# Performance work log

Measured on AMD Instinct MI355X. Metric: run time of the kernel, lower is better.

Reference implementation:

```python
import jax, jax.numpy as jnp
import numpy as np

L, D, H, IMG, P, B, E = 12, 768, 12, 224, 16, 32, 512
HD = D // H            # 64
FF = 4 * D             # 3072
SEQ = (IMG // P) ** 2 + 1  # 197


def _ln(x, w, b, eps=1e-5):
    m = x.mean(-1, keepdims=True)
    v = jnp.mean((x - m) ** 2, axis=-1, keepdims=True)
    return (x - m) * jax.lax.rsqrt(v + eps) * w + b


def setup_inputs() -> dict:
    key = jax.random.key(0)
    ks = jax.random.split(key, 10)
    r = lambda k, shape, s=0.02: (jax.random.normal(k, shape, jnp.float32) * s)
    return {
        'image': jax.random.normal(ks[0], (B, 3, IMG, IMG), jnp.float32),
        'conv_w': r(ks[1], (D, 3, P, P)),
        'cls_emb': r(ks[2], (D,)),
        'pos_emb': r(ks[3], (SEQ, D)),
        'ln_pre_w': jnp.ones((D,), jnp.float32), 'ln_pre_b': jnp.zeros((D,), jnp.float32),
        'ln1_w': jnp.ones((L, D), jnp.float32), 'ln1_b': jnp.zeros((L, D), jnp.float32),
        'qkv_w': r(ks[4], (L, 3 * D, D)), 'qkv_b': jnp.zeros((L, 3 * D), jnp.float32),
        'out_w': r(ks[5], (L, D, D)), 'out_b': jnp.zeros((L, D), jnp.float32),
        'ln2_w': jnp.ones((L, D), jnp.float32), 'ln2_b': jnp.zeros((L, D), jnp.float32),
        'fc_w': r(ks[6], (L, FF, D)), 'fc_b': jnp.zeros((L, FF), jnp.float32),
        'pr_w': r(ks[7], (L, D, FF)), 'pr_b': jnp.zeros((L, D), jnp.float32),
        'ln_post_w': jnp.ones((D,), jnp.float32), 'ln_post_b': jnp.zeros((D,), jnp.float32),
        'proj': r(ks[8], (D, E)),
    }


def reference(image, conv_w, cls_emb, pos_emb, ln_pre_w, ln_pre_b,
              ln1_w, ln1_b, qkv_w, qkv_b, out_w, out_b,
              ln2_w, ln2_b, fc_w, fc_b, pr_w, pr_b,
              ln_post_w, ln_post_b, proj):
    # patchify: conv stride=kernel=patch, no bias -> [B, D, 14, 14]
    x = jax.lax.conv_general_dilated(image, conv_w, (P, P), 'VALID',
                                     dimension_numbers=('NCHW', 'OIHW', 'NCHW'))
    x = x.reshape(B, D, -1).transpose(0, 2, 1)               # [B, 196, D]
    cls = jnp.broadcast_to(cls_emb, (B, 1, D))
    x = jnp.concatenate([cls, x], axis=1) + pos_emb          # [B, SEQ, D]
    x = _ln(x, ln_pre_w, ln_pre_b)
    x = x.transpose(1, 0, 2)                                  # [SEQ, B, D]
    scale = 1.0 / np.sqrt(HD).astype(np.float32)

    def step(x, p):
        l1w, l1b, qw, qb, ow, ob, l2w, l2b, fw, fb, pw, pb = p
        h = _ln(x, l1w, l1b)
        qkv = h @ qw.T + qb                                    # [SEQ, B, 3D]
        q, k, v = jnp.split(qkv, 3, axis=-1)
        heads = lambda t: t.reshape(SEQ, B * H, HD).transpose(1, 0, 2)  # [B*H, SEQ, HD]
        q = heads(q) * scale
        k = heads(k)
        v = heads(v)
        a = jax.nn.softmax(jnp.einsum('nsh,nth->nst', q, k), axis=-1)   # [B*H, SEQ, SEQ]
        o = jnp.einsum('nst,nth->nsh', a, v)                  # [B*H, SEQ, HD]
        o = o.transpose(1, 0, 2).reshape(SEQ, B, D)
        x = x + (o @ ow.T + ob)
        h = _ln(x, l2w, l2b)
        h = jax.nn.gelu(h @ fw.T + fb, approximate=False)      # torch nn.GELU (exact)
        x = x + (h @ pw.T + pb)
        return x, None

    x, _ = jax.lax.scan(step, x, (ln1_w, ln1_b, qkv_w, qkv_b, out_w, out_b,
                                  ln2_w, ln2_b, fc_w, fc_b, pr_w, pr_b))
    x = x.transpose(1, 0, 2)                                   # [B, SEQ, D]
    cls_tok = _ln(x[:, 0, :], ln_post_w, ln_post_b)
    feats = cls_tok @ proj                                     # [B, E]
    return feats / jnp.linalg.norm(feats, axis=-1, keepdims=True)
```

## Files before the change

kernel.cpp:

```cpp
#include <hip/hip_runtime.h>
#include <stdint.h>

#define SEQ 197
#define NB 32
#define NH 12
#define NTOK (SEQ*NB)
#define MPAD 6400
#define NPATCH 6272

typedef unsigned short u16;
typedef unsigned int u32;
typedef __attribute__((ext_vector_type(8))) short bv8;
typedef __attribute__((ext_vector_type(4))) float f32x4;

__device__ __forceinline__ u16 f2bf(float f){
  u32 u = __float_as_uint(f);
  u = (u + 0x7fffu + ((u >> 16) & 1u)) >> 16;
  return (u16)u;
}
__device__ __forceinline__ float bf2f(u16 h){ return __uint_as_float(((u32)h) << 16); }

#if defined(__has_builtin)
#if __has_builtin(__builtin_amdgcn_global_load_lds)
#define HAS_GLLDS 1
#endif
#endif

__device__ __forceinline__ void gl_lds16(const void* g, void* l){
#ifdef HAS_GLLDS
  __builtin_amdgcn_global_load_lds(
      (const __attribute__((address_space(1))) void*)(uintptr_t)g,
      (__attribute__((address_space(3))) void*)(u32)(uintptr_t)l, 16, 0, 0);
#else
  int lane = threadIdx.x & 63;
  uint4 v = *(const uint4*)((const char*)g);
  *(uint4*)((char*)l + lane*16) = v;
#endif
}

__device__ __forceinline__ void red2(float& a, float& b){
  #pragma unroll
  for (int o = 32; o > 0; o >>= 1){ a += __shfl_down(a, o); b += __shfl_down(b, o); }
  __shared__ float red[8];
  int w = threadIdx.x >> 6, ln = threadIdx.x & 63;
  if (ln == 0){ red[w] = a; red[4 + w] = b; }
  __syncthreads();
  a = red[0] + red[1] + red[2] + red[3];
  b = red[4] + red[5] + red[6] + red[7];
}

__global__ __launch_bounds__(256) void cvt_k(const float* __restrict__ src, u16* __restrict__ dst, int n4){
  int i = blockIdx.x * 256 + threadIdx.x;
  if (i >= n4) return;
  float4 f = ((const float4*)src)[i];
  u32 lo = (u32)f2bf(f.x) | ((u32)f2bf(f.y) << 16);
  u32 hi = (u32)f2bf(f.z) | ((u32)f2bf(f.w) << 16);
  ((uint2*)dst)[i] = make_uint2(lo, hi);
}

__global__ __launch_bounds__(256) void im2col_k(const float* __restrict__ img, u16* __restrict__ Ap){
  int gid = blockIdx.x * 256 + threadIdx.x;
  int row = gid / 768, k = gid - row * 768;
  int b = row / 196, p = row - b * 196;
  int pr = p / 14, pc = p - pr * 14;
  int c = k >> 8, r = k & 255;
  int ph = r >> 4, pw = r & 15;
  size_t src = ((size_t)(b * 3 + c) * 224 + (pr * 16 + ph)) * 224 + (pc * 16 + pw);
  Ap[gid] = f2bf(img[src]);
}

template<int EPI>
__global__ __launch_bounds__(256, 2)
void gemm_2ph(const u16* __restrict__ A, const u16* __restrict__ Bw,
              const float* __restrict__ bias, float* __restrict__ Cf,
              u16* __restrict__ Cb, int N, int K, int Mreal,
              int RM, int RN, int tmT, int tnT)
{
  __shared__ __align__(16) u16 sA0[128 * 64];
  __shared__ __align__(16) u16 sB0[128 * 64];
  __shared__ __align__(16) u16 sA1[128 * 64];
  __shared__ __align__(16) u16 sB1[128 * 64];
  const int xcd = blockIdx.x & 7, pos = blockIdx.x >> 3;
  const int xm = xcd >> 1, xn = xcd & 1;
  const int tm = xm * RM + pos / RN;
  const int tn = xn * RN + pos % RN;
  if (tm >= tmT || tn >= tnT) return;

  const int tid = threadIdx.x;
  const int lane = tid & 63, wave = tid >> 6;
  const int wm = wave >> 1, wn = wave & 1;
  const int lr = lane & 15, g = lane >> 4, g4 = g * 4;
  const int KT = K >> 6;

  const int srow = lane >> 3;
  const int sch = (lane & 7) ^ srow;
  const u16* aB[4]; const u16* bB[4];
  #pragma unroll
  for (int j = 0; j < 4; j++){
    int rr = wave * 32 + j * 8;
    aB[j] = A  + (size_t)(tm * 128 + rr + srow) * K + sch * 8;
    bB[j] = Bw + (size_t)(tn * 128 + rr + srow) * K + sch * 8;
  }

  f32x4 acc[4][4] = {};

  auto stage = [&](int kt, u16* dA, u16* dB){
    #pragma unroll
    for (int j = 0; j < 4; j++)
      gl_lds16(aB[j] + (size_t)kt * 64, dA + (wave * 32 + j * 8) * 64);
    #pragma unroll
    for (int j = 0; j < 4; j++)
      gl_lds16(bB[j] + (size_t)kt * 64, dB + (wave * 32 + j * 8) * 64);
  };
  auto tile = [&](const u16* sA, const u16* sB, u16* dA, u16* dB, int ktNext, bool doStage, bool last){
    if (last) asm volatile("s_waitcnt vmcnt(0)" ::: "memory");
    else      asm volatile("s_waitcnt vmcnt(8)" ::: "memory");
    __builtin_amdgcn_s_barrier();
    bv8 af[4][2], bf[4][2];
    #pragma unroll
    for (int mi = 0; mi < 4; mi++){
      int row = wm * 64 + mi * 16 + lr;
      #pragma unroll
      for (int kk = 0; kk < 2; kk++)
        af[mi][kk] = *(const bv8*)((const char*)sA + row * 128 + ((kk * 64 + g * 16) ^ ((row & 7) << 4)));
    }
    #pragma unroll
    for (int ni = 0; ni < 4; ni++){
      int row = wn * 64 + ni * 16 + lr;
      #pragma unroll
      for (int kk = 0; kk < 2; kk++)
        bf[ni][kk] = *(const bv8*)((const char*)sB + row * 128 + ((kk * 64 + g * 16) ^ ((row & 7) << 4)));
    }
    asm volatile("s_waitcnt lgkmcnt(0)" ::: "memory");
    __builtin_amdgcn_s_barrier();
    if (doStage) stage(ktNext, dA, dB);
    __builtin_amdgcn_s_setprio(1);
    #pragma unroll
    for (int kk = 0; kk < 2; kk++)
      #pragma unroll
      for (int mi = 0; mi < 4; mi++)
        #pragma unroll
        for (int ni = 0; ni < 4; ni++)
          acc[mi][ni] = __builtin_amdgcn_mfma_f32_16x16x32_bf16(af[mi][kk], bf[ni][kk], acc[mi][ni], 0, 0, 0);
    __builtin_amdgcn_s_setprio(0);
  };

  stage(0, sA0, sB0);
  stage(1, sA1, sB1);
  int t = 0;
  for (; t + 2 < KT; t += 2){
    tile(sA0, sB0, sA0, sB0, t + 2, true,  false);
    tile(sA1, sB1, sA1, sB1, t + 3, true,  false);
  }
  tile(sA0, sB0, sA0, sB0, 0, false, false);
  tile(sA1, sB1, sA1, sB1, 0, false, true);

  if (EPI == 1 || EPI == 3){
    __syncthreads();
    #pragma unroll
    for (int mi = 0; mi < 4; mi++){
      #pragma unroll
      for (int ni = 0; ni < 4; ni++){
        int bcol = wn * 64 + ni * 16 + lr;
        float bvs = bias[tn * 128 + bcol];
        #pragma unroll
        for (int j = 0; j < 4; j++){
          int brow = wm * 64 + mi * 16 + g4 + j;
          float v = acc[mi][ni][j] + bvs;
          if (EPI == 3) v = 0.5f * v * (1.f + erff(v * 0.70710678118654752f));
          char* base = (char*)(brow < 64 ? sA0 : sB0);
          *(u16*)(base + (brow & 63) * 256 + ((bcol * 2) ^ ((brow & 7) << 4))) = f2bf(v);
        }
      }
    }
    __syncthreads();
    #pragma unroll
    for (int c = 0; c < 8; c++){
      int off = c * 4096 + tid * 16;
      int row = off >> 8;
      int colb = off & 255;
      const char* base = (const char*)(row < 64 ? sA0 : sB0);
      uint4 v = *(const uint4*)(base + (row & 63) * 256 + (colb ^ ((row & 7) << 4)));
      *(uint4*)((char*)(Cb + (size_t)(tm * 128 + row) * N + tn * 128) + colb) = v;
    }
  } else {
    #pragma unroll
    for (int ni = 0; ni < 4; ni++){
      int col = tn * 128 + wn * 64 + ni * 16 + lr;
      float bvs = (EPI != 0) ? bias[col] : 0.f;
      #pragma unroll
      for (int mi = 0; mi < 4; mi++){
        int row0 = tm * 128 + wm * 64 + mi * 16 + g4;
        #pragma unroll
        for (int j = 0; j < 4; j++){
          int row = row0 + j;
          if (row < Mreal){
            float v = acc[mi][ni][j] + bvs;
            size_t idx = (size_t)row * N + col;
            if (EPI == 0) Cf[idx] = v;
            else          Cf[idx] += v;
          }
        }
      }
    }
  }
}

__global__ __launch_bounds__(256, 1) void attn_k(const u16* __restrict__ qkv, u16* __restrict__ o_out){
  __shared__ __align__(16) u16 sK[256 * 64];
  __shared__ __align__(16) u16 sVT[64 * 256];
  __shared__ __align__(16) u16 sP[4 * 64 * 64];
  const int bh = blockIdx.x;
  const int b = bh / NH, h = bh - b * NH;
  const int tid = threadIdx.x;
  const int lane = tid & 63, wave = tid >> 6;
  const int lr = lane & 15, g = lane >> 4;
  const int g4 = g * 4;
  const int wb = wave * 64;
  const u16* kbase = qkv + (size_t)b * SEQ * 2304 + h * 64 + 768;
  const u16* vbase = kbase + 768;

  bv8 qf[4][2];
  #pragma unroll
  for (int qt = 0; qt < 4; qt++){
    int q = wb + qt * 16 + lr; if (q > 196) q = 196;
    const u16* qr = qkv + (size_t)(b * SEQ + q) * 2304 + h * 64;
    #pragma unroll
    for (int kc = 0; kc < 2; kc++)
      qf[qt][kc] = *(const bv8*)(qr + kc * 32 + g * 8);
  }

  for (int i = tid; i < 197 * 32; i += 256){
    int r = i >> 5, c = i & 31;
    u32 kv_ = *(const u32*)(kbase + (size_t)r * 2304 + c * 2);
    *(u32*)((char*)sK + ((r * 128 + c * 4) ^ ((r & 7) << 4))) = kv_;
    u32 vv = *(const u32*)(vbase + (size_t)r * 2304 + c * 2);
    int hd0 = c * 2, hd1 = c * 2 + 1;
    *(u16*)((char*)sVT + ((hd0 * 512 + r * 2) ^ ((hd0 & 7) << 4))) = (u16)(vv & 0xffff);
    *(u16*)((char*)sVT + ((hd1 * 512 + r * 2) ^ ((hd1 & 7) << 4))) = (u16)(vv >> 16);
  }
  for (int i = tid; i < 59 * 32; i += 256){
    int r = 197 + (i >> 5), c = i & 31;
    *(u32*)((char*)sK + (r * 128 + c * 4)) = 0;
  }
  for (int i = tid; i < 59 * 64; i += 256){
    int kv = 197 + (i >> 6), hd = i & 63;
    *(u16*)((char*)sVT + ((hd * 512 + kv * 2) ^ ((hd & 7) << 4))) = 0;
  }
  __syncthreads();

  f32x4 acc_o[4][4] = {};
  float m_[4] = {-1e30f, -1e30f, -1e30f, -1e30f};
  float l_[4] = {0.f, 0.f, 0.f, 0.f};
  u16* sPw = sP + wave * 4096;

  for (int ch = 0; ch < 4; ++ch){
    f32x4 st[4][4] = {};
    #pragma unroll
    for (int kc = 0; kc < 2; kc++){
      bv8 kf[4];
      #pragma unroll
      for (int kvt = 0; kvt < 4; kvt++){
        int row = ch * 64 + kvt * 16 + lr;
        kf[kvt] = *(const bv8*)((const char*)sK + ((row * 128 + kc * 64 + g * 16) ^ ((row & 7) << 4)));
      }
      #pragma unroll
      for (int kvt = 0; kvt < 4; kvt++)
        #pragma unroll
        for (int qt = 0; qt < 4; qt++)
          st[kvt][qt] = __builtin_amdgcn_mfma_f32_16x16x32_bf16(kf[kvt], qf[qt][kc], st[kvt][qt], 0, 0, 0);
    }
    float fac[4];
    #pragma unroll
    for (int qt = 0; qt < 4; qt++){
      float mx = -1e30f;
      #pragma unroll
      for (int kvt = 0; kvt < 4; kvt++)
        #pragma unroll
        for (int j = 0; j < 4; j++){
          int kvg = ch * 64 + kvt * 16 + g4 + j;
          float s = st[kvt][qt][j] * 0.125f;
          s = (kvg < 197) ? s : -1e30f;
          st[kvt][qt][j] = s;
          mx = fmaxf(mx, s);
        }
      mx = fmaxf(mx, __shfl_xor(mx, 16));
      mx = fmaxf(mx, __shfl_xor(mx, 32));
      float nm = fmaxf(m_[qt], mx);
      fac[qt] = __expf(m_[qt] - nm);
      m_[qt] = nm;
      float ls = 0.f;
      #pragma unroll
      for (int kvt = 0; kvt < 4; kvt++)
        #pragma unroll
        for (int j = 0; j < 4; j++){
          float p = __expf(st[kvt][qt][j] - nm);
          st[kvt][qt][j] = p;
          ls += p;
        }
      ls += __shfl_xor(ls, 16);
      ls += __shfl_xor(ls, 32);
      l_[qt] = l_[qt] * fac[qt] + ls;
    }
    #pragma unroll
    for (int qt = 0; qt < 4; qt++)
      #pragma unroll
      for (int j = 0; j < 4; j++){
        float fj = __shfl(fac[qt], (lane & 48) | (g4 + j));
        #pragma unroll
        for (int nt = 0; nt < 4; nt++) acc_o[qt][nt][j] *= fj;
      }
    #pragma unroll
    for (int qt = 0; qt < 4; qt++){
      int row = qt * 16 + lr;
      #pragma unroll
      for (int kvt = 0; kvt < 4; kvt++){
        uint2 pk;
        pk.x = (u32)f2bf(st[kvt][qt][0]) | ((u32)f2bf(st[kvt][qt][1]) << 16);
        pk.y = (u32)f2bf(st[kvt][qt][2]) | ((u32)f2bf(st[kvt][qt][3]) << 16);
        *(uint2*)((char*)sPw + ((row * 128 + kvt * 32 + g * 8) ^ ((row & 7) << 4))) = pk;
      }
    }
    #pragma unroll
    for (int kc = 0; kc < 2; kc++){
      bv8 pa[4], vb[4];
      #pragma unroll
      for (int qt = 0; qt < 4; qt++){
        int row = qt * 16 + lr;
        pa[qt] = *(const bv8*)((const char*)sPw + ((row * 128 + kc * 64 + g * 16) ^ ((row & 7) << 4)));
      }
      #pragma unroll
      for (int nt = 0; nt < 4; nt++){
        int hd = nt * 16 + lr;
        vb[nt] = *(const bv8*)((const char*)sVT + ((hd * 512 + ch * 128 + kc * 64 + g * 16) ^ ((hd & 7) << 4)));
      }
      #pragma unroll
      for (int qt = 0; qt < 4; qt++)
        #pragma unroll
        for (int nt = 0; nt < 4; nt++)
          acc_o[qt][nt] = __builtin_amdgcn_mfma_f32_16x16x32_bf16(pa[qt], vb[nt], acc_o[qt][nt], 0, 0, 0);
    }
  }

  #pragma unroll
  for (int qt = 0; qt < 4; qt++)
    #pragma unroll
    for (int j = 0; j < 4; j++){
      float lj = __shfl(l_[qt], (lane & 48) | (g4 + j));
      float rl = 1.f / lj;
      int row = wb + qt * 16 + g4 + j;
      if (row < 197){
        u16* dst = o_out + (size_t)(b * SEQ + row) * 768 + h * 64;
        #pragma unroll
        for (int nt = 0; nt < 4; nt++)
          dst[nt * 16 + lr] = f2bf(acc_o[qt][nt][j] * rl);
      }
    }
}

__global__ __launch_bounds__(256) void embed_ln_k(const float* __restrict__ patch, const float* __restrict__ cls,
    const float* __restrict__ pos, const float* __restrict__ w, const float* __restrict__ bb, float* __restrict__ x)
{
  int t = blockIdx.x;
  int b = t / SEQ, s = t - b * SEQ;
  int tid = threadIdx.x;
  float v[3];
  #pragma unroll
  for (int i = 0; i < 3; i++){
    int d = tid + i * 256;
    float base = (s == 0) ? cls[d] : patch[(size_t)(b * 196 + s - 1) * 768 + d];
    v[i] = base + pos[s * 768 + d];
  }
  float sm = v[0] + v[1] + v[2];
  float sq = v[0]*v[0] + v[1]*v[1] + v[2]*v[2];
  red2(sm, sq);
  float m = sm * (1.f / 768.f);
  float rs = rsqrtf(sq * (1.f / 768.f) - m * m + 1e-5f);
  #pragma unroll
  for (int i = 0; i < 3; i++){
    int d = tid + i * 256;
    x[(size_t)t * 768 + d] = (v[i] - m) * rs * w[d] + bb[d];
  }
}

__global__ __launch_bounds__(256) void ln_bf16_k(const float* __restrict__ x, const float* __restrict__ w,
    const float* __restrict__ bb, u16* __restrict__ h)
{
  int t = blockIdx.x, tid = threadIdx.x;
  const float* xr = x + (size_t)t * 768;
  float v[3];
  #pragma unroll
  for (int i = 0; i < 3; i++) v[i] = xr[tid + i * 256];
  float sm = v[0] + v[1] + v[2];
  float sq = v[0]*v[0] + v[1]*v[1] + v[2]*v[2];
  red2(sm, sq);
  float m = sm * (1.f / 768.f);
  float rs = rsqrtf(sq * (1.f / 768.f) - m * m + 1e-5f);
  #pragma unroll
  for (int i = 0; i < 3; i++){
    int d = tid + i * 256;
    h[(size_t)t * 768 + d] = f2bf((v[i] - m) * rs * w[d] + bb[d]);
  }
}

__global__ __launch_bounds__(256) void ln_cls_k(const float* __restrict__ x, const float* __restrict__ w,
    const float* __restrict__ bb, float* __restrict__ cls)
{
  int b = blockIdx.x, tid = threadIdx.x;
  const float* xr = x + (size_t)b * SEQ * 768;
  float v[3];
  #pragma unroll
  for (int i = 0; i < 3; i++) v[i] = xr[tid + i * 256];
  float sm = v[0] + v[1] + v[2];
  float sq = v[0]*v[0] + v[1]*v[1] + v[2]*v[2];
  red2(sm, sq);
  float m = sm * (1.f / 768.f);
  float rs = rsqrtf(sq * (1.f / 768.f) - m * m + 1e-5f);
  #pragma unroll
  for (int i = 0; i < 3; i++){
    int d = tid + i * 256;
    cls[b * 768 + d] = (v[i] - m) * rs * w[d] + bb[d];
  }
}

__global__ __launch_bounds__(256) void proj_k(const float* __restrict__ cls, const float* __restrict__ P,
                                              float* __restrict__ feats){
  int gid = blockIdx.x * 256 + threadIdx.x;
  int b = gid >> 9, e = gid & 511;
  const float* c = cls + b * 768;
  float a0 = 0, a1 = 0, a2 = 0, a3 = 0;
  for (int d = 0; d < 768; d += 4){
    a0 += c[d]     * P[(size_t)d * 512 + e];
    a1 += c[d + 1] * P[(size_t)(d + 1) * 512 + e];
    a2 += c[d + 2] * P[(size_t)(d + 2) * 512 + e];
    a3 += c[d + 3] * P[(size_t)(d + 3) * 512 + e];
  }
  feats[gid] = (a0 + a1) + (a2 + a3);
}

__global__ __launch_bounds__(256) void norm_k(const float* __restrict__ feats, float* __restrict__ out){
  int b = blockIdx.x, tid = threadIdx.x;
  float v0 = feats[b * 512 + tid], v1 = feats[b * 512 + 256 + tid];
  float sq = v0 * v0 + v1 * v1, dummy = 0.f;
  red2(sq, dummy);
  float inv = 1.f / sqrtf(sq);
  out[b * 512 + tid] = v0 * inv;
  out[b * 512 + 256 + tid] = v1 * inv;
}

extern "C" void kernel_launch(void* const* d_in, const int* in_sizes, int n_in,
                              void* d_out, int out_size, void* d_ws, size_t ws_size,
                              hipStream_t stream)
{
  const float* image   = (const float*)d_in[0];
  const float* conv_w  = (const float*)d_in[1];
  const float* cls_emb = (const float*)d_in[2];
  const float* pos_emb = (const float*)d_in[3];
  const float* lnprew  = (const float*)d_in[4];
  const float* lnpreb  = (const float*)d_in[5];
  const float* ln1w    = (const float*)d_in[6];
  const float* ln1b    = (const float*)d_in[7];
  const float* qkvw    = (const float*)d_in[8];
  const float* qkvb    = (const float*)d_in[9];
  const float* outw    = (const float*)d_in[10];
  const float* outb    = (const float*)d_in[11];
  const float* ln2w    = (const float*)d_in[12];
  const float* ln2b    = (const float*)d_in[13];
  const float* fcw     = (const float*)d_in[14];
  const float* fcb     = (const float*)d_in[15];
  const float* prw     = (const float*)d_in[16];
  const float* prb     = (const float*)d_in[17];
  const float* lnpostw = (const float*)d_in[18];
  const float* lnpostb = (const float*)d_in[19];
  const float* proj    = (const float*)d_in[20];
  (void)in_sizes; (void)n_in; (void)out_size;

  const size_t QW = (size_t)2304 * 768, OW = (size_t)768 * 768;
  const size_t FW = (size_t)3072 * 768, PW = (size_t)768 * 3072;
  const size_t CW = (size_t)768 * 768;

  char* p = (char*)d_ws;
  auto alloc = [&](size_t bytes)->char*{ char* r = p; p += (bytes + 255) & ~(size_t)255; return r; };
  float* x     = (float*)alloc((size_t)MPAD * 768 * 4);
  u16*   h     = (u16*)  alloc((size_t)MPAD * 768 * 2);
  u16*   qkvB  = (u16*)  alloc((size_t)MPAD * 2304 * 2);
  u16*   attno = (u16*)  alloc((size_t)MPAD * 768 * 2);
  u16*   ffh   = (u16*)  alloc((size_t)MPAD * 3072 * 2);
  u16*   Ap    = (u16*)  alloc((size_t)NPATCH * 768 * 2);
  float* patch = (float*)alloc((size_t)NPATCH * 768 * 4);
  float* clsb  = (float*)alloc((size_t)32 * 768 * 4);
  float* feats = (float*)alloc((size_t)32 * 512 * 4);
  u16*   cwb   = (u16*)  alloc(CW * 2);
  size_t base_used = (size_t)(p - (char*)d_ws);
  size_t full_need = (QW + OW + FW + PW) * 12 * 2;
  bool full = (base_used + full_need + 4096 <= ws_size);

  u16 *wq = nullptr, *wo = nullptr, *wf = nullptr, *wp = nullptr;
  u16 *sq_ = nullptr, *so_ = nullptr, *sf_ = nullptr, *sp_ = nullptr;
  if (full){
    wq = (u16*)alloc(QW * 12 * 2); wo = (u16*)alloc(OW * 12 * 2);
    wf = (u16*)alloc(FW * 12 * 2); wp = (u16*)alloc(PW * 12 * 2);
  } else {
    sq_ = (u16*)alloc(QW * 2); so_ = (u16*)alloc(OW * 2);
    sf_ = (u16*)alloc(FW * 2); sp_ = (u16*)alloc(PW * 2);
  }
  if ((size_t)(p - (char*)d_ws) > ws_size) return;

  { int n4 = (int)(CW / 4); cvt_k<<<(n4 + 255) / 256, 256, 0, stream>>>(conv_w, cwb, n4); }
  if (full){
    int n4;
    n4 = (int)(QW * 12 / 4); cvt_k<<<(n4 + 255) / 256, 256, 0, stream>>>(qkvw, wq, n4);
    n4 = (int)(OW * 12 / 4); cvt_k<<<(n4 + 255) / 256, 256, 0, stream>>>(outw, wo, n4);
    n4 = (int)(FW * 12 / 4); cvt_k<<<(n4 + 255) / 256, 256, 0, stream>>>(fcw,  wf, n4);
    n4 = (int)(PW * 12 / 4); cvt_k<<<(n4 + 255) / 256, 256, 0, stream>>>(prw,  wp, n4);
  }

  im2col_k<<<(NPATCH * 768) / 256, 256, 0, stream>>>(image, Ap);
  gemm_2ph<0><<<8 * 13 * 3, 256, 0, stream>>>(Ap, cwb, nullptr, patch, nullptr, 768, 768, NPATCH, 13, 3, 49, 6);
  embed_ln_k<<<NTOK, 256, 0, stream>>>(patch, cls_emb, pos_emb, lnprew, lnpreb, x);

  for (int l = 0; l < 12; l++){
    const u16 *WQ, *WO, *WF, *WP;
    if (full){
      WQ = wq + (size_t)l * QW; WO = wo + (size_t)l * OW;
      WF = wf + (size_t)l * FW; WP = wp + (size_t)l * PW;
    } else {
      int n4;
      n4 = (int)(QW / 4); cvt_k<<<(n4 + 255) / 256, 256, 0, stream>>>(qkvw + (size_t)l * QW, sq_, n4);
      n4 = (int)(OW / 4); cvt_k<<<(n4 + 255) / 256, 256, 0, stream>>>(outw + (size_t)l * OW, so_, n4);
      n4 = (int)(FW / 4); cvt_k<<<(n4 + 255) / 256, 256, 0, stream>>>(fcw  + (size_t)l * FW, sf_, n4);
      n4 = (int)(PW / 4); cvt_k<<<(n4 + 255) / 256, 256, 0, stream>>>(prw  + (size_t)l * PW, sp_, n4);
      WQ = sq_; WO = so_; WF = sf_; WP = sp_;
    }
    ln_bf16_k<<<NTOK, 256, 0, stream>>>(x, ln1w + l * 768, ln1b + l * 768, h);
    gemm_2ph<1><<<8 * 13 * 9, 256, 0, stream>>>(h, WQ, qkvb + l * 2304, nullptr, qkvB, 2304, 768, NTOK, 13, 9, 50, 18);
    attn_k<<<NB * NH, 256, 0, stream>>>(qkvB, attno);
    gemm_2ph<2><<<8 * 13 * 3, 256, 0, stream>>>(attno, WO, outb + l * 768, x, nullptr, 768, 768, NTOK, 13, 3, 50, 6);
    ln_bf16_k<<<NTOK, 256, 0, stream>>>(x, ln2w + l * 768, ln2b + l * 768, h);
    gemm_2ph<3><<<8 * 13 * 12, 256, 0, stream>>>(h, WF, fcb + l * 3072, nullptr, ffh, 3072, 768, NTOK, 13, 12, 50, 24);
    gemm_2ph<2><<<8 * 13 * 3, 256, 0, stream>>>(ffh, WP, prb + l * 768, x, nullptr, 768, 3072, NTOK, 13, 3, 50, 6);
  }

  ln_cls_k<<<NB, 256, 0, stream>>>(x, lnpostw, lnpostb, clsb);
  proj_k<<<(NB * 512) / 256, 256, 0, stream>>>(clsb, proj, feats);
  norm_k<<<NB, 256, 0, stream>>>(feats, (float*)d_out);
}
```

Baseline: 2.911 ms.

## Add 256x256-tile double-buffered GEMM for QKV and FC projections

```diff
diff --git a/kernel.cpp b/kernel.cpp
--- a/kernel.cpp
+++ b/kernel.cpp
@@ -203,6 +203,122 @@
         }
       }
     }
+  }
+}
+
+template<int EPI>
+__global__ __launch_bounds__(512, 2)
+void gemm_256(const u16* __restrict__ A, const u16* __restrict__ Bw,
+              const float* __restrict__ bias, u16* __restrict__ Cb,
+              int N, int K, int gx)
+{
+  __shared__ __align__(16) u16 sA0[256 * 64];
+  __shared__ __align__(16) u16 sB0[256 * 64];
+  __shared__ __align__(16) u16 sA1[256 * 64];
+  __shared__ __align__(16) u16 sB1[256 * 64];
+  const int nwg = gridDim.x;
+  const int q = nwg >> 3, r = nwg & 7;
+  const int xcd = blockIdx.x & 7, pos = blockIdx.x >> 3;
+  const int wg = (xcd < r ? xcd * (q + 1) : r * (q + 1) + (xcd - r) * q) + pos;
+  const int tm = wg / gx, tn = wg - tm * gx;
+
+  const int tid = threadIdx.x;
+  const int lane = tid & 63, wave = tid >> 6;
+  const int wm = wave >> 2, wn = wave & 3;
+  const int lr = lane & 15, g = lane >> 4, g4 = g * 4;
+  const int KT = K >> 6;
+
+  const int srow = lane >> 3;
+  const int sch = (lane & 7) ^ srow;
+  const u16* aB[4]; const u16* bB[4];
+  #pragma unroll
+  for (int j = 0; j < 4; j++){
+    int rr = wave * 32 + j * 8;
+    aB[j] = A  + (size_t)(tm * 256 + rr + srow) * K + sch * 8;
+    bB[j] = Bw + (size_t)(tn * 256 + rr + srow) * K + sch * 8;
+  }
+
+  f32x4 acc[8][4] = {};
+
+  auto stage = [&](int kt, u16* dA, u16* dB){
+    #pragma unroll
+    for (int j = 0; j < 4; j++)
+      gl_lds16(aB[j] + (size_t)kt * 64, dA + (wave * 32 + j * 8) * 64);
+    #pragma unroll
+    for (int j = 0; j < 4; j++)
+      gl_lds16(bB[j] + (size_t)kt * 64, dB + (wave * 32 + j * 8) * 64);
+  };
+  auto tile = [&](const u16* sA, const u16* sB, u16* dA, u16* dB, int ktNext, bool doStage, bool last){
+    if (last) asm volatile("s_waitcnt vmcnt(0)" ::: "memory");
+    else      asm volatile("s_waitcnt vmcnt(8)" ::: "memory");
+    __builtin_amdgcn_s_barrier();
+    bv8 af[8][2], bf[4][2];
+    #pragma unroll
+    for (int mi = 0; mi < 8; mi++){
+      int row = wm * 128 + mi * 16 + lr;
+      #pragma unroll
+      for (int kk = 0; kk < 2; kk++)
+        af[mi][kk] = *(const bv8*)((const char*)sA + row * 128 + ((kk * 64 + g * 16) ^ ((row & 7) << 4)));
+    }
+    #pragma unroll
+    for (int ni = 0; ni < 4; ni++){
+      int row = wn * 64 + ni * 16 + lr;
+      #pragma unroll
+      for (int kk = 0; kk < 2; kk++)
+        bf[ni][kk] = *(const bv8*)((const char*)sB + row * 128 + ((kk * 64 + g * 16) ^ ((row & 7) << 4)));
+    }
+    asm volatile("s_waitcnt lgkmcnt(0)" ::: "memory");
+    __builtin_amdgcn_s_barrier();
+    if (doStage) stage(ktNext, dA, dB);
+    __builtin_amdgcn_s_setprio(1);
+    #pragma unroll
+    for (int kk = 0; kk < 2; kk++)
+      #pragma unroll
+      for (int mi = 0; mi < 8; mi++)
+        #pragma unroll
+        for (int ni = 0; ni < 4; ni++)
+          acc[mi][ni] = __builtin_amdgcn_mfma_f32_16x16x32_bf16(af[mi][kk], bf[ni][kk], acc[mi][ni], 0, 0, 0);
+    __builtin_amdgcn_s_setprio(0);
+  };
+
+  stage(0, sA0, sB0);
+  stage(1, sA1, sB1);
+  int t = 0;
+  for (; t + 2 < KT; t += 2){
+    tile(sA0, sB0, sA0, sB0, t + 2, true,  false);
+    tile(sA1, sB1, sA1, sB1, t + 3, true,  false);
+  }
+  tile(sA0, sB0, sA0, sB0, 0, false, false);
+  tile(sA1, sB1, sA1, sB1, 0, false, true);
+
+  __syncthreads();
+  #pragma unroll
+  for (int mi = 0; mi < 8; mi++){
+    #pragma unroll
+    for (int ni = 0; ni < 4; ni++){
+      int bcol = wn * 64 + ni * 16 + lr;
+      float bvs = bias[tn * 256 + bcol];
+      #pragma unroll
+      for (int j = 0; j < 4; j++){
+        int brow = wm * 128 + mi * 16 + g4 + j;
+        float v = acc[mi][ni][j] + bvs;
+        if (EPI == 3) v = 0.5f * v * (1.f + erff(v * 0.70710678118654752f));
+        int sel = brow >> 6;
+        char* base = (char*)(sel == 0 ? sA0 : sel == 1 ? sB0 : sel == 2 ? sA1 : sB1);
+        *(u16*)(base + (brow & 63) * 512 + ((bcol * 2) ^ ((brow & 7) << 4))) = f2bf(v);
+      }
+    }
+  }
+  __syncthreads();
+  #pragma unroll
+  for (int c = 0; c < 16; c++){
+    int off = c * 8192 + tid * 16;
+    int row = off >> 9;
+    int colb = off & 511;
+    int sel = row >> 6;
+    const char* base = (const char*)(sel == 0 ? sA0 : sel == 1 ? sB0 : sel == 2 ? sA1 : sB1);
+    uint4 v = *(const uint4*)(base + (row & 63) * 512 + (colb ^ ((row & 7) << 4)));
+    *(uint4*)((char*)(Cb + (size_t)(tm * 256 + row) * N + tn * 256) + colb) = v;
   }
 }
 
@@ -533,11 +649,11 @@
       WQ = sq_; WO = so_; WF = sf_; WP = sp_;
     }
     ln_bf16_k<<<NTOK, 256, 0, stream>>>(x, ln1w + l * 768, ln1b + l * 768, h);
-    gemm_2ph<1><<<8 * 13 * 9, 256, 0, stream>>>(h, WQ, qkvb + l * 2304, nullptr, qkvB, 2304, 768, NTOK, 13, 9, 50, 18);
+    gemm_256<1><<<25 * 9, 512, 0, stream>>>(h, WQ, qkvb + l * 2304, qkvB, 2304, 768, 9);
     attn_k<<<NB * NH, 256, 0, stream>>>(qkvB, attno);
     gemm_2ph<2><<<8 * 13 * 3, 256, 0, stream>>>(attno, WO, outb + l * 768, x, nullptr, 768, 768, NTOK, 13, 3, 50, 6);
     ln_bf16_k<<<NTOK, 256, 0, stream>>>(x, ln2w + l * 768, ln2b + l * 768, h);
-    gemm_2ph<3><<<8 * 13 * 12, 256, 0, stream>>>(h, WF, fcb + l * 3072, nullptr, ffh, 3072, 768, NTOK, 13, 12, 50, 24);
+    gemm_256<3><<<25 * 12, 512, 0, stream>>>(h, WF, fcb + l * 3072, ffh, 3072, 768, 12);
     gemm_2ph<2><<<8 * 13 * 3, 256, 0, stream>>>(ffh, WP, prb + l * 768, x, nullptr, 768, 3072, NTOK, 13, 3, 50, 6);
   }
 
```

After: 4.914 ms. +68.8%, slower.

## Add single-buffered GEMM variant with higher occupancy for short-K GEMMs

Applied to the files above, without the earlier changes.

```diff
diff --git a/kernel.cpp b/kernel.cpp
--- a/kernel.cpp
+++ b/kernel.cpp
@@ -70,7 +70,121 @@
 }
 
 template<int EPI>
-__global__ __launch_bounds__(256, 2)
+__global__ __launch_bounds__(256, 8)
+void gemm_sw(const u16* __restrict__ A, const u16* __restrict__ Bw,
+             const float* __restrict__ bias, float* __restrict__ Cf,
+             u16* __restrict__ Cb, int N, int K, int Mreal,
+             int RM, int RN, int tmT, int tnT)
+{
+  __shared__ __align__(16) u16 sA[128 * 64];
+  __shared__ __align__(16) u16 sB[128 * 64];
+  const int xcd = blockIdx.x & 7, pos = blockIdx.x >> 3;
+  const int xm = xcd >> 1, xn = xcd & 1;
+  const int tm = xm * RM + pos / RN;
+  const int tn = xn * RN + pos % RN;
+  if (tm >= tmT || tn >= tnT) return;
+
+  const int tid = threadIdx.x;
+  const int lane = tid & 63, wave = tid >> 6;
+  const int wm = wave >> 1, wn = wave & 1;
+  const int lr = lane & 15, g = lane >> 4, g4 = g * 4;
+  const int KT = K >> 6;
+
+  const int srow = lane >> 3;
+  const int sch = (lane & 7) ^ srow;
+  const u16* aB[4]; const u16* bB[4];
+  u16* lA[4]; u16* lB[4];
+  #pragma unroll
+  for (int j = 0; j < 4; j++){
+    int rr = wave * 32 + j * 8;
+    aB[j] = A  + (size_t)(tm * 128 + rr + srow) * K + sch * 8;
+    bB[j] = Bw + (size_t)(tn * 128 + rr + srow) * K + sch * 8;
+    lA[j] = sA + rr * 64;
+    lB[j] = sB + rr * 64;
+  }
+
+  f32x4 acc[4][4] = {};
+
+  for (int kt = 0; kt < KT; ++kt){
+    __syncthreads();
+    #pragma unroll
+    for (int j = 0; j < 4; j++) gl_lds16(aB[j] + (size_t)kt * 64, lA[j]);
+    #pragma unroll
+    for (int j = 0; j < 4; j++) gl_lds16(bB[j] + (size_t)kt * 64, lB[j]);
+    __syncthreads();
+    #pragma unroll
+    for (int kk = 0; kk < 2; kk++){
+      bv8 af[4], bf[4];
+      #pragma unroll
+      for (int mi = 0; mi < 4; mi++){
+        int row = wm * 64 + mi * 16 + lr;
+        af[mi] = *(const bv8*)((const char*)sA + row * 128 + ((kk * 64 + g * 16) ^ ((row & 7) << 4)));
+      }
+      #pragma unroll
+      for (int ni = 0; ni < 4; ni++){
+        int row = wn * 64 + ni * 16 + lr;
+        bf[ni] = *(const bv8*)((const char*)sB + row * 128 + ((kk * 64 + g * 16) ^ ((row & 7) << 4)));
+      }
+      #pragma unroll
+      for (int mi = 0; mi < 4; mi++)
+        #pragma unroll
+        for (int ni = 0; ni < 4; ni++)
+          acc[mi][ni] = __builtin_amdgcn_mfma_f32_16x16x32_bf16(af[mi], bf[ni], acc[mi][ni], 0, 0, 0);
+    }
+  }
+
+  if (EPI == 1 || EPI == 3){
+    __syncthreads();
+    u16* sC = sA;
+    #pragma unroll
+    for (int mi = 0; mi < 4; mi++){
+      #pragma unroll
+      for (int ni = 0; ni < 4; ni++){
+        int bcol = wn * 64 + ni * 16 + lr;
+        float bvs = bias[tn * 128 + bcol];
+        #pragma unroll
+        for (int j = 0; j < 4; j++){
+          int brow = wm * 64 + mi * 16 + g4 + j;
+          float v = acc[mi][ni][j] + bvs;
+          if (EPI == 3) v = 0.5f * v * (1.f + erff(v * 0.70710678118654752f));
+          *(u16*)((char*)sC + brow * 256 + ((bcol * 2) ^ ((brow & 7) << 4))) = f2bf(v);
+        }
+      }
+    }
+    __syncthreads();
+    #pragma unroll
+    for (int c = 0; c < 8; c++){
+      int off = c * 4096 + tid * 16;
+      int row = off >> 8;
+      int colb = off & 255;
+      uint4 v = *(const uint4*)((const char*)sC + row * 256 + (colb ^ ((row & 7) << 4)));
+      *(uint4*)((char*)(Cb + (size_t)(tm * 128 + row) * N + tn * 128) + colb) = v;
+    }
+  } else {
+    #pragma unroll
+    for (int ni = 0; ni < 4; ni++){
+      int col = tn * 128 + wn * 64 + ni * 16 + lr;
+      float bvs = (EPI != 0) ? bias[col] : 0.f;
+      #pragma unroll
+      for (int mi = 0; mi < 4; mi++){
+        int row0 = tm * 128 + wm * 64 + mi * 16 + g4;
+        #pragma unroll
+        for (int j = 0; j < 4; j++){
+          int row = row0 + j;
+          if (row < Mreal){
+            float v = acc[mi][ni][j] + bvs;
+            size_t idx = (size_t)row * N + col;
+            if (EPI == 0) Cf[idx] = v;
+            else          Cf[idx] += v;
+          }
+        }
+      }
+    }
+  }
+}
+
+template<int EPI>
+__global__ __launch_bounds__(256, 4)
 void gemm_2ph(const u16* __restrict__ A, const u16* __restrict__ Bw,
               const float* __restrict__ bias, float* __restrict__ Cf,
               u16* __restrict__ Cb, int N, int K, int Mreal,
@@ -516,7 +630,7 @@
   }
 
   im2col_k<<<(NPATCH * 768) / 256, 256, 0, stream>>>(image, Ap);
-  gemm_2ph<0><<<8 * 13 * 3, 256, 0, stream>>>(Ap, cwb, nullptr, patch, nullptr, 768, 768, NPATCH, 13, 3, 49, 6);
+  gemm_sw<0><<<8 * 13 * 3, 256, 0, stream>>>(Ap, cwb, nullptr, patch, nullptr, 768, 768, NPATCH, 13, 3, 49, 6);
   embed_ln_k<<<NTOK, 256, 0, stream>>>(patch, cls_emb, pos_emb, lnprew, lnpreb, x);
 
   for (int l = 0; l < 12; l++){
@@ -533,11 +647,11 @@
       WQ = sq_; WO = so_; WF = sf_; WP = sp_;
     }
     ln_bf16_k<<<NTOK, 256, 0, stream>>>(x, ln1w + l * 768, ln1b + l * 768, h);
-    gemm_2ph<1><<<8 * 13 * 9, 256, 0, stream>>>(h, WQ, qkvb + l * 2304, nullptr, qkvB, 2304, 768, NTOK, 13, 9, 50, 18);
+    gemm_sw<1><<<8 * 13 * 9, 256, 0, stream>>>(h, WQ, qkvb + l * 2304, nullptr, qkvB, 2304, 768, NTOK, 13, 9, 50, 18);
     attn_k<<<NB * NH, 256, 0, stream>>>(qkvB, attno);
-    gemm_2ph<2><<<8 * 13 * 3, 256, 0, stream>>>(attno, WO, outb + l * 768, x, nullptr, 768, 768, NTOK, 13, 3, 50, 6);
+    gemm_sw<2><<<8 * 13 * 3, 256, 0, stream>>>(attno, WO, outb + l * 768, x, nullptr, 768, 768, NTOK, 13, 3, 50, 6);
     ln_bf16_k<<<NTOK, 256, 0, stream>>>(x, ln2w + l * 768, ln2b + l * 768, h);
-    gemm_2ph<3><<<8 * 13 * 12, 256, 0, stream>>>(h, WF, fcb + l * 3072, nullptr, ffh, 3072, 768, NTOK, 13, 12, 50, 24);
+    gemm_sw<3><<<8 * 13 * 12, 256, 0, stream>>>(h, WF, fcb + l * 3072, nullptr, ffh, 3072, 768, NTOK, 13, 12, 50, 24);
     gemm_2ph<2><<<8 * 13 * 3, 256, 0, stream>>>(ffh, WP, prb + l * 768, x, nullptr, 768, 3072, NTOK, 13, 3, 50, 6);
   }
 
```

Result: slower. 3.269 ms (+12.3%).
